# Performance work log

Hardware: AMD Instinct MI355X
Metric: run time of the kernel (lower is better)

## Reference

```python
import jax, jax.numpy as jnp
import numpy as np
from jax.scipy.linalg import expm

LATENT, HID, OMEGA, TRANZ, K = 64, 40, 9, 3, 262144


def _linear_params(key, out_d, in_d):
    # equinox Linear default init: U(-1/sqrt(in), 1/sqrt(in)) for weight and bias
    lim = 1.0 / np.sqrt(in_d)
    kw, kb = jax.random.split(key)
    W = jax.random.uniform(kw, (out_d, in_d), minval=-lim, maxval=lim, dtype=jnp.float32)
    b = jax.random.uniform(kb, (out_d,), minval=-lim, maxval=lim, dtype=jnp.float32)
    return W, b


def setup_inputs() -> dict:
    key = jax.random.key(0)
    keys = jax.random.split(key, 7)
    W_o1, b_o1 = _linear_params(keys[0], HID, LATENT)
    W_o2, b_o2 = _linear_params(keys[1], HID, HID)
    W_o3, b_o3 = _linear_params(keys[2], OMEGA, HID)
    W_t1, b_t1 = _linear_params(keys[3], HID, LATENT)
    W_t2, b_t2 = _linear_params(keys[4], HID, HID)
    W_t3, b_t3 = _linear_params(keys[5], TRANZ, HID)
    x = jax.random.normal(keys[6], (LATENT, K), dtype=jnp.float32)
    return {
        "x": x,
        "W_o1": W_o1, "b_o1": b_o1, "W_o2": W_o2, "b_o2": b_o2, "W_o3": W_o3, "b_o3": b_o3,
        "W_t1": W_t1, "b_t1": b_t1, "W_t2": W_t2, "b_t2": b_t2, "W_t3": W_t3, "b_t3": b_t3,
    }


def _exp_omega(omega_flat):
    # omega_flat: (9, K); expm of each column reshaped to 3x3, flattened -> (K, 9)
    f = lambda col: expm(col.reshape(3, 3)).reshape(9)
    return jax.vmap(f, in_axes=1)(omega_flat)


def reference(x, W_o1, b_o1, W_o2, b_o2, W_o3, b_o3,
              W_t1, b_t1, W_t2, b_t2, W_t3, b_t3):
    relu = jax.nn.relu
    # omega branch (note: original applies relu after EVERY layer, incl. last)
    h = relu(W_o1 @ x + b_o1[:, None])
    h = relu(W_o2 @ h + b_o2[:, None])
    omega = relu(W_o3 @ h + b_o3[:, None])          # (9, K)
    rotation = _exp_omega(omega).T                   # (9, K)
    # translation branch
    t = relu(W_t1 @ x + b_t1[:, None])
    t = relu(W_t2 @ t + b_t2[:, None])
    translation = relu(W_t3 @ t + b_t3[:, None])     # (3, K)
    return (omega, rotation, translation)
```

## Files before the change

kernel.cpp:

```cpp
#include <hip/hip_runtime.h>
#include <hip/hip_bf16.h>

#define KC 262144

typedef __attribute__((ext_vector_type(8))) short bf16x8;
typedef __attribute__((ext_vector_type(4))) float f32x4;
typedef unsigned short u16;
typedef unsigned int u32;

__device__ __forceinline__ u16 f2bf(float f) {
    u32 u = __float_as_uint(f);
    return (u16)((u + 0x7fffu + ((u >> 16) & 1u)) >> 16);
}
__device__ __forceinline__ u32 pk2(float a, float b) {
    return (u32)f2bf(a) | ((u32)f2bf(b) << 16);
}
__device__ __forceinline__ float bf2f(u32 h) {
    return __uint_as_float(h << 16);
}

__global__ __launch_bounds__(256) void prep(
    const float* __restrict__ Wo1, const float* __restrict__ bo1,
    const float* __restrict__ Wo2, const float* __restrict__ bo2,
    const float* __restrict__ Wo3, const float* __restrict__ bo3,
    const float* __restrict__ Wt1, const float* __restrict__ bt1,
    const float* __restrict__ Wt2, const float* __restrict__ bt2,
    const float* __restrict__ Wt3, const float* __restrict__ bt3,
    u16* __restrict__ ws)
{
    u16* W1s = ws;
    u16* W2s = ws + 5120;
    u16* W3s = ws + 12800;
    float* b1s = (float*)(ws + 14336);
    const int t0 = blockIdx.x * 256 + threadIdx.x;
    const int NT = gridDim.x * 256;

    for (int i = t0; i < 5120; i += NT) {
        int r = i >> 6, k = i & 63;
        float v = (r < 40) ? Wo1[r * 64 + k] : Wt1[(r - 40) * 64 + k];
        W1s[i] = f2bf(v);
    }
    for (int i = t0; i < 7680; i += NT) {
        int r = i / 96, k = i - r * 96;
        float v = 0.f;
        if (r < 40) {
            if (k < 40) v = Wo2[r * 40 + k];
            else if (k == 80) v = bo2[r];
        } else {
            int rr = r - 40;
            if (k >= 40 && k < 80) v = Wt2[rr * 40 + (k - 40)];
            else if (k == 80) v = bt2[rr];
        }
        W2s[i] = f2bf(v);
    }
    for (int i = t0; i < 1536; i += NT) {
        int r = i / 96, k = i - r * 96;
        float v = 0.f;
        if (r < 9) {
            if (k < 40) v = Wo3[r * 40 + k];
            else if (k == 80) v = bo3[r];
        } else if (r < 12) {
            int rr = r - 9;
            if (k >= 40 && k < 80) v = Wt3[rr * 40 + (k - 40)];
            else if (k == 80) v = bt3[rr];
        }
        W3s[i] = f2bf(v);
    }
    for (int i = t0; i < 80; i += NT)
        b1s[i] = (i < 40) ? bo1[i] : bt1[i - 40];
}

__global__ __launch_bounds__(256, 2) void mlp_mfma(
    const float* __restrict__ x, const u16* __restrict__ ws,
    float* __restrict__ out)
{
    const u16* W1s = ws;
    const u16* W2s = ws + 5120;
    const u16* W3s = ws + 12800;
    const float* b1s = (const float*)(ws + 14336);

    __shared__ u16 hst[4][16][120];
    __shared__ u16 l3s[4][64][18];

    const int tid = threadIdx.x;
    const int wid = tid >> 6;
    const int lane = tid & 63;
    const int g = lane >> 4;
    const int c = lane & 15;
    const int wgid = blockIdx.x * 4 + wid;
    const int cbase = wgid * 64;

    bf16x8 A1[5][2], A3[3];
    f32x4 b1v[5];
#pragma unroll
    for (int m = 0; m < 5; ++m) {
#pragma unroll
        for (int s = 0; s < 2; ++s)
            A1[m][s] = *(const bf16x8*)(W1s + (16 * m + c) * 64 + 32 * s + 8 * g);
        b1v[m] = *(const f32x4*)(b1s + 16 * m + 4 * g);
    }
    bf16x8 A2[5][3];
#pragma unroll
    for (int m = 0; m < 5; ++m)
#pragma unroll
        for (int s = 0; s < 3; ++s)
            if (!(s == 0 && m >= 3))
                A2[m][s] = *(const bf16x8*)(W2s + (16 * m + c) * 96 + 32 * s + 8 * g);
#pragma unroll
    for (int s = 0; s < 3; ++s)
        A3[s] = *(const bf16x8*)(W3s + c * 96 + 32 * s + 8 * g);

    {
        uint2 z;
        z.x = (g == 0) ? 0x00003f80u : 0u;
        z.y = 0u;
        *(uint2*)&hst[wid][c][80 + 4 * g] = z;
    }

    u32 xoff[16];
#pragma unroll
    for (int jj = 0; jj < 16; ++jj) {
        int row = 8 * g + (jj & 7) + 32 * (jj >> 3);
        xoff[jj] = (u32)((row * KC + cbase + c) * 4);
    }
    const char* xb_ = (const char*)x;

#pragma unroll
    for (int t = 0; t < 4; ++t) {
        float xr[16];
#pragma unroll
        for (int jj = 0; jj < 16; ++jj)
            xr[jj] = *(const float*)(xb_ + (xoff[jj] + t * 64));
        bf16x8 xv[2];
#pragma unroll
        for (int s = 0; s < 2; ++s) {
            union { u32 u[4]; bf16x8 v; } uu;
#pragma unroll
            for (int p = 0; p < 4; ++p)
                uu.u[p] = pk2(xr[8 * s + 2 * p], xr[8 * s + 2 * p + 1]);
            xv[s] = uu.v;
        }

        f32x4 a1[5];
#pragma unroll
        for (int m = 0; m < 5; ++m) a1[m] = b1v[m];
#pragma unroll
        for (int s = 0; s < 2; ++s)
#pragma unroll
            for (int m = 0; m < 5; ++m)
                a1[m] = __builtin_amdgcn_mfma_f32_16x16x32_bf16(
                    A1[m][s], xv[s], a1[m], 0, 0, 0);
#pragma unroll
        for (int m = 0; m < 5; ++m) {
            uint2 w;
            w.x = pk2(fmaxf(a1[m][0], 0.f), fmaxf(a1[m][1], 0.f));
            w.y = pk2(fmaxf(a1[m][2], 0.f), fmaxf(a1[m][3], 0.f));
            *(uint2*)&hst[wid][c][16 * m + 4 * g] = w;
        }

        f32x4 a2[5];
#pragma unroll
        for (int m = 0; m < 5; ++m) a2[m] = f32x4{0.f, 0.f, 0.f, 0.f};
#pragma unroll
        for (int s = 0; s < 3; ++s) {
            bf16x8 hb = *(const bf16x8*)&hst[wid][c][32 * s + 8 * g];
#pragma unroll
            for (int m = 0; m < 5; ++m)
                if (!(s == 0 && m >= 3))
                    a2[m] = __builtin_amdgcn_mfma_f32_16x16x32_bf16(
                        A2[m][s], hb, a2[m], 0, 0, 0);
        }
#pragma unroll
        for (int m = 0; m < 5; ++m) {
            uint2 w;
            w.x = pk2(fmaxf(a2[m][0], 0.f), fmaxf(a2[m][1], 0.f));
            w.y = pk2(fmaxf(a2[m][2], 0.f), fmaxf(a2[m][3], 0.f));
            *(uint2*)&hst[wid][c][16 * m + 4 * g] = w;
        }

        f32x4 a3 = f32x4{0.f, 0.f, 0.f, 0.f};
#pragma unroll
        for (int s = 0; s < 3; ++s) {
            bf16x8 hb = *(const bf16x8*)&hst[wid][c][32 * s + 8 * g];
            a3 = __builtin_amdgcn_mfma_f32_16x16x32_bf16(
                A3[s], hb, a3, 0, 0, 0);
        }
        {
            uint2 w;
            w.x = pk2(fmaxf(a3[0], 0.f), fmaxf(a3[1], 0.f));
            w.y = pk2(fmaxf(a3[2], 0.f), fmaxf(a3[3], 0.f));
            *(uint2*)&l3s[wid][16 * t + c][4 * g] = w;
        }
    }

    {
        uint4 q0 = *(const uint4*)&l3s[wid][lane][0];
        uint2 q1 = *(const uint2*)&l3s[wid][lane][8];
        float om[9];
        om[0] = bf2f(q0.x & 0xffffu); om[1] = bf2f(q0.x >> 16);
        om[2] = bf2f(q0.y & 0xffffu); om[3] = bf2f(q0.y >> 16);
        om[4] = bf2f(q0.z & 0xffffu); om[5] = bf2f(q0.z >> 16);
        om[6] = bf2f(q0.w & 0xffffu); om[7] = bf2f(q0.w >> 16);
        om[8] = bf2f(q1.x & 0xffffu);
        float tr0 = bf2f(q1.x >> 16);
        float tr1 = bf2f(q1.y & 0xffffu);
        float tr2 = bf2f(q1.y >> 16);

        const size_t ob = (size_t)cbase + lane;
#pragma unroll
        for (int j = 0; j < 9; ++j)
            out[(size_t)j * KC + ob] = om[j];
        out[(size_t)18 * KC + ob] = tr0;
        out[(size_t)19 * KC + ob] = tr1;
        out[(size_t)20 * KC + ob] = tr2;

        float B[9];
#pragma unroll
        for (int i = 0; i < 9; ++i) B[i] = om[i] * (1.0f / 32.0f);
        float T[9] = {1.f, 0.f, 0.f, 0.f, 1.f, 0.f, 0.f, 0.f, 1.f};
#pragma unroll
        for (int m = 9; m >= 1; --m) {
            float U[9];
#pragma unroll
            for (int rr = 0; rr < 3; ++rr)
#pragma unroll
                for (int cc = 0; cc < 3; ++cc)
                    U[rr * 3 + cc] = B[rr * 3 + 0] * T[0 * 3 + cc]
                                   + B[rr * 3 + 1] * T[1 * 3 + cc]
                                   + B[rr * 3 + 2] * T[2 * 3 + cc];
            const float s = 1.0f / (float)m;
#pragma unroll
            for (int i = 0; i < 9; ++i)
                T[i] = U[i] * s + ((i == 0 || i == 4 || i == 8) ? 1.0f : 0.0f);
        }
#pragma unroll
        for (int q = 0; q < 5; ++q) {
            float U[9];
#pragma unroll
            for (int rr = 0; rr < 3; ++rr)
#pragma unroll
                for (int cc = 0; cc < 3; ++cc)
                    U[rr * 3 + cc] = T[rr * 3 + 0] * T[0 * 3 + cc]
                                   + T[rr * 3 + 1] * T[1 * 3 + cc]
                                   + T[rr * 3 + 2] * T[2 * 3 + cc];
#pragma unroll
            for (int i = 0; i < 9; ++i) T[i] = U[i];
        }
#pragma unroll
        for (int j = 0; j < 9; ++j)
            out[(size_t)(9 + j) * KC + ob] = T[j];
    }
}

extern "C" void kernel_launch(void* const* d_in, const int* in_sizes, int n_in,
                              void* d_out, int out_size, void* d_ws, size_t ws_size,
                              hipStream_t stream) {
    const float* x   = (const float*)d_in[0];
    const float* Wo1 = (const float*)d_in[1];
    const float* bo1 = (const float*)d_in[2];
    const float* Wo2 = (const float*)d_in[3];
    const float* bo2 = (const float*)d_in[4];
    const float* Wo3 = (const float*)d_in[5];
    const float* bo3 = (const float*)d_in[6];
    const float* Wt1 = (const float*)d_in[7];
    const float* bt1 = (const float*)d_in[8];
    const float* Wt2 = (const float*)d_in[9];
    const float* bt2 = (const float*)d_in[10];
    const float* Wt3 = (const float*)d_in[11];
    const float* bt3 = (const float*)d_in[12];

    u16* ws = (u16*)d_ws;
    float* out = (float*)d_out;

    hipLaunchKernelGGL(prep, dim3(16), dim3(256), 0, stream,
                       Wo1, bo1, Wo2, bo2, Wo3, bo3,
                       Wt1, bt1, Wt2, bt2, Wt3, bt3, ws);
    hipLaunchKernelGGL(mlp_mfma, dim3(1024), dim3(256), 0, stream,
                       x, ws, out);
}
```

Measured before the change: 34.41 us.

## Stage x through LDS with float4 loads and shuffle layer-3 outputs

Replaces the per-lane scalar 4-byte strided loads of x with coalesced float4 global loads staged into a shared slab, from which the MFMA B operands are gathered. Layer-3 results are now redistributed across lanes with warp shuffles instead of an extra LDS buffer, and the hidden-state buffer aliases the x staging slab. The hand-written bf16 rounding is swapped for the library conversion. The aim is wider memory transactions and a smaller LDS footprint, at the cost of extra LDS traffic, shuffle instructions and more registers held live.

```diff
diff --git a/kernel.cpp b/kernel.cpp
--- a/kernel.cpp
+++ b/kernel.cpp
@@ -13,7 +13,9 @@
     return (u16)((u + 0x7fffu + ((u >> 16) & 1u)) >> 16);
 }
 __device__ __forceinline__ u32 pk2(float a, float b) {
-    return (u32)f2bf(a) | ((u32)f2bf(b) << 16);
+    u16 lo = __bfloat16_as_ushort(__float2bfloat16(a));
+    u16 hi = __bfloat16_as_ushort(__float2bfloat16(b));
+    return (u32)lo | ((u32)hi << 16);
 }
 __device__ __forceinline__ float bf2f(u32 h) {
     return __uint_as_float(h << 16);
@@ -79,8 +81,7 @@
     const u16* W3s = ws + 12800;
     const float* b1s = (const float*)(ws + 14336);
 
-    __shared__ u16 hst[4][16][120];
-    __shared__ u16 l3s[4][64][18];
+    __shared__ float slab[4][64 * 36];
 
     const int tid = threadIdx.x;
     const int wid = tid >> 6;
@@ -90,6 +91,9 @@
     const int wgid = blockIdx.x * 4 + wid;
     const int cbase = wgid * 64;
 
+    float* xstage = &slab[wid][0];
+    u16* hstp = (u16*)&slab[wid][0];
+
     bf16x8 A1[5][2], A3[3];
     f32x4 b1v[5];
 #pragma unroll
@@ -110,101 +114,129 @@
     for (int s = 0; s < 3; ++s)
         A3[s] = *(const bf16x8*)(W3s + c * 96 + 32 * s + 8 * g);
 
+    const char* gbase = (const char*)x
+        + ((size_t)(lane >> 3) * KC + (size_t)(cbase + 4 * (lane & 7))) * 4;
+    const int wb = (lane >> 3) * 36 + 4 * (lane & 7);
+
+    u32 w0[4], w1[4];
+
+#pragma unroll
+    for (int ch = 0; ch < 2; ++ch) {
+        float4 G[8];
+#pragma unroll
+        for (int i = 0; i < 8; ++i)
+            G[i] = *(const float4*)(gbase + (size_t)i * 8 * KC * 4 + ch * 128);
+#pragma unroll
+        for (int i = 0; i < 8; ++i)
+            *(float4*)&xstage[wb + i * 288] = G[i];
+
+        bf16x8 xv[2][2];
+#pragma unroll
+        for (int tl = 0; tl < 2; ++tl)
+#pragma unroll
+            for (int s = 0; s < 2; ++s) {
+                union { u32 u[4]; bf16x8 v; } uu;
+#pragma unroll
+                for (int p = 0; p < 4; ++p) {
+                    float lo = xstage[(8 * g + 32 * s + 2 * p) * 36 + 16 * tl + c];
+                    float hi = xstage[(8 * g + 32 * s + 2 * p + 1) * 36 + 16 * tl + c];
+                    uu.u[p] = pk2(lo, hi);
+                }
+                xv[tl][s] = uu.v;
+            }
+
+        {
+            uint2 z;
+            z.x = (g == 0) ? 0x00003f80u : 0u;
+            z.y = 0u;
+            *(uint2*)&hstp[c * 120 + 80 + 4 * g] = z;
+        }
+
+#pragma unroll
+        for (int tl = 0; tl < 2; ++tl) {
+            const int gt = 2 * ch + tl;
+
+            f32x4 a1[5];
+#pragma unroll
+            for (int m = 0; m < 5; ++m) a1[m] = b1v[m];
+#pragma unroll
+            for (int s = 0; s < 2; ++s)
+#pragma unroll
+                for (int m = 0; m < 5; ++m)
+                    a1[m] = __builtin_amdgcn_mfma_f32_16x16x32_bf16(
+                        A1[m][s], xv[tl][s], a1[m], 0, 0, 0);
+#pragma unroll
+            for (int m = 0; m < 5; ++m) {
+                uint2 w;
+                w.x = pk2(fmaxf(a1[m][0], 0.f), fmaxf(a1[m][1], 0.f));
+                w.y = pk2(fmaxf(a1[m][2], 0.f), fmaxf(a1[m][3], 0.f));
+                *(uint2*)&hstp[c * 120 + 16 * m + 4 * g] = w;
+            }
+
+            f32x4 a2[5];
+#pragma unroll
+            for (int m = 0; m < 5; ++m) a2[m] = f32x4{0.f, 0.f, 0.f, 0.f};
+#pragma unroll
+            for (int s = 0; s < 3; ++s) {
+                bf16x8 hb = *(const bf16x8*)&hstp[c * 120 + 32 * s + 8 * g];
+#pragma unroll
+                for (int m = 0; m < 5; ++m)
+                    if (!(s == 0 && m >= 3))
+                        a2[m] = __builtin_amdgcn_mfma_f32_16x16x32_bf16(
+                            A2[m][s], hb, a2[m], 0, 0, 0);
+            }
+#pragma unroll
+            for (int m = 0; m < 5; ++m) {
+                uint2 w;
+                w.x = pk2(fmaxf(a2[m][0], 0.f), fmaxf(a2[m][1], 0.f));
+                w.y = pk2(fmaxf(a2[m][2], 0.f), fmaxf(a2[m][3], 0.f));
+                *(uint2*)&hstp[c * 120 + 16 * m + 4 * g] = w;
+            }
+
+            f32x4 a3 = f32x4{0.f, 0.f, 0.f, 0.f};
+#pragma unroll
+            for (int s = 0; s < 3; ++s) {
+                bf16x8 hb = *(const bf16x8*)&hstp[c * 120 + 32 * s + 8 * g];
+                a3 = __builtin_amdgcn_mfma_f32_16x16x32_bf16(
+                    A3[s], hb, a3, 0, 0, 0);
+            }
+            w0[gt] = pk2(fmaxf(a3[0], 0.f), fmaxf(a3[1], 0.f));
+            w1[gt] = pk2(fmaxf(a3[2], 0.f), fmaxf(a3[3], 0.f));
+        }
+    }
+
     {
-        uint2 z;
-        z.x = (g == 0) ? 0x00003f80u : 0u;
-        z.y = 0u;
-        *(uint2*)&hst[wid][c][80 + 4 * g] = z;
-    }
-
-    u32 xoff[16];
-#pragma unroll
-    for (int jj = 0; jj < 16; ++jj) {
-        int row = 8 * g + (jj & 7) + 32 * (jj >> 3);
-        xoff[jj] = (u32)((row * KC + cbase + c) * 4);
-    }
-    const char* xb_ = (const char*)x;
-
-#pragma unroll
-    for (int t = 0; t < 4; ++t) {
-        float xr[16];
-#pragma unroll
-        for (int jj = 0; jj < 16; ++jj)
-            xr[jj] = *(const float*)(xb_ + (xoff[jj] + t * 64));
-        bf16x8 xv[2];
-#pragma unroll
-        for (int s = 0; s < 2; ++s) {
-            union { u32 u[4]; bf16x8 v; } uu;
-#pragma unroll
-            for (int p = 0; p < 4; ++p)
-                uu.u[p] = pk2(xr[8 * s + 2 * p], xr[8 * s + 2 * p + 1]);
-            xv[s] = uu.v;
-        }
-
-        f32x4 a1[5];
-#pragma unroll
-        for (int m = 0; m < 5; ++m) a1[m] = b1v[m];
-#pragma unroll
-        for (int s = 0; s < 2; ++s)
-#pragma unroll
-            for (int m = 0; m < 5; ++m)
-                a1[m] = __builtin_amdgcn_mfma_f32_16x16x32_bf16(
-                    A1[m][s], xv[s], a1[m], 0, 0, 0);
-#pragma unroll
-        for (int m = 0; m < 5; ++m) {
-            uint2 w;
-            w.x = pk2(fmaxf(a1[m][0], 0.f), fmaxf(a1[m][1], 0.f));
-            w.y = pk2(fmaxf(a1[m][2], 0.f), fmaxf(a1[m][3], 0.f));
-            *(uint2*)&hst[wid][c][16 * m + 4 * g] = w;
-        }
-
-        f32x4 a2[5];
-#pragma unroll
-        for (int m = 0; m < 5; ++m) a2[m] = f32x4{0.f, 0.f, 0.f, 0.f};
-#pragma unroll
-        for (int s = 0; s < 3; ++s) {
-            bf16x8 hb = *(const bf16x8*)&hst[wid][c][32 * s + 8 * g];
-#pragma unroll
-            for (int m = 0; m < 5; ++m)
-                if (!(s == 0 && m >= 3))
-                    a2[m] = __builtin_amdgcn_mfma_f32_16x16x32_bf16(
-                        A2[m][s], hb, a2[m], 0, 0, 0);
-        }
-#pragma unroll
-        for (int m = 0; m < 5; ++m) {
-            uint2 w;
-            w.x = pk2(fmaxf(a2[m][0], 0.f), fmaxf(a2[m][1], 0.f));
-            w.y = pk2(fmaxf(a2[m][2], 0.f), fmaxf(a2[m][3], 0.f));
-            *(uint2*)&hst[wid][c][16 * m + 4 * g] = w;
-        }
-
-        f32x4 a3 = f32x4{0.f, 0.f, 0.f, 0.f};
-#pragma unroll
-        for (int s = 0; s < 3; ++s) {
-            bf16x8 hb = *(const bf16x8*)&hst[wid][c][32 * s + 8 * g];
-            a3 = __builtin_amdgcn_mfma_f32_16x16x32_bf16(
-                A3[s], hb, a3, 0, 0, 0);
-        }
-        {
-            uint2 w;
-            w.x = pk2(fmaxf(a3[0], 0.f), fmaxf(a3[1], 0.f));
-            w.y = pk2(fmaxf(a3[2], 0.f), fmaxf(a3[3], 0.f));
-            *(uint2*)&l3s[wid][16 * t + c][4 * g] = w;
-        }
-    }
-
-    {
-        uint4 q0 = *(const uint4*)&l3s[wid][lane][0];
-        uint2 q1 = *(const uint2*)&l3s[wid][lane][8];
+        const int T = lane >> 4;
+        const int cp = lane & 15;
+        const int s0 = cp, s1 = 16 + cp, s2 = 32 + cp;
+
+        auto selT = [&](u32 v0, u32 v1, u32 v2, u32 v3) -> u32 {
+            u32 lo = (T & 1) ? v1 : v0;
+            u32 hi = (T & 1) ? v3 : v2;
+            return (T & 2) ? hi : lo;
+        };
+        u32 q0 = selT((u32)__shfl((int)w0[0], s0), (u32)__shfl((int)w0[1], s0),
+                      (u32)__shfl((int)w0[2], s0), (u32)__shfl((int)w0[3], s0));
+        u32 q1 = selT((u32)__shfl((int)w1[0], s0), (u32)__shfl((int)w1[1], s0),
+                      (u32)__shfl((int)w1[2], s0), (u32)__shfl((int)w1[3], s0));
+        u32 q2 = selT((u32)__shfl((int)w0[0], s1), (u32)__shfl((int)w0[1], s1),
+                      (u32)__shfl((int)w0[2], s1), (u32)__shfl((int)w0[3], s1));
+        u32 q3 = selT((u32)__shfl((int)w1[0], s1), (u32)__shfl((int)w1[1], s1),
+                      (u32)__shfl((int)w1[2], s1), (u32)__shfl((int)w1[3], s1));
+        u32 q4 = selT((u32)__shfl((int)w0[0], s2), (u32)__shfl((int)w0[1], s2),
+                      (u32)__shfl((int)w0[2], s2), (u32)__shfl((int)w0[3], s2));
+        u32 q5 = selT((u32)__shfl((int)w1[0], s2), (u32)__shfl((int)w1[1], s2),
+                      (u32)__shfl((int)w1[2], s2), (u32)__shfl((int)w1[3], s2));
+
         float om[9];
-        om[0] = bf2f(q0.x & 0xffffu); om[1] = bf2f(q0.x >> 16);
-        om[2] = bf2f(q0.y & 0xffffu); om[3] = bf2f(q0.y >> 16);
-        om[4] = bf2f(q0.z & 0xffffu); om[5] = bf2f(q0.z >> 16);
-        om[6] = bf2f(q0.w & 0xffffu); om[7] = bf2f(q0.w >> 16);
-        om[8] = bf2f(q1.x & 0xffffu);
-        float tr0 = bf2f(q1.x >> 16);
-        float tr1 = bf2f(q1.y & 0xffffu);
-        float tr2 = bf2f(q1.y >> 16);
+        om[0] = bf2f(q0 & 0xffffu); om[1] = bf2f(q0 >> 16);
+        om[2] = bf2f(q1 & 0xffffu); om[3] = bf2f(q1 >> 16);
+        om[4] = bf2f(q2 & 0xffffu); om[5] = bf2f(q2 >> 16);
+        om[6] = bf2f(q3 & 0xffffu); om[7] = bf2f(q3 >> 16);
+        om[8] = bf2f(q4 & 0xffffu);
+        float tr0 = bf2f(q4 >> 16);
+        float tr1 = bf2f(q5 & 0xffffu);
+        float tr2 = bf2f(q5 >> 16);
 
         const size_t ob = (size_t)cbase + lane;
 #pragma unroll
@@ -217,7 +249,7 @@
         float B[9];
 #pragma unroll
         for (int i = 0; i < 9; ++i) B[i] = om[i] * (1.0f / 32.0f);
-        float T[9] = {1.f, 0.f, 0.f, 0.f, 1.f, 0.f, 0.f, 0.f, 1.f};
+        float T9[9] = {1.f, 0.f, 0.f, 0.f, 1.f, 0.f, 0.f, 0.f, 1.f};
 #pragma unroll
         for (int m = 9; m >= 1; --m) {
             float U[9];
@@ -225,13 +257,13 @@
             for (int rr = 0; rr < 3; ++rr)
 #pragma unroll
                 for (int cc = 0; cc < 3; ++cc)
-                    U[rr * 3 + cc] = B[rr * 3 + 0] * T[0 * 3 + cc]
-                                   + B[rr * 3 + 1] * T[1 * 3 + cc]
-                                   + B[rr * 3 + 2] * T[2 * 3 + cc];
+                    U[rr * 3 + cc] = B[rr * 3 + 0] * T9[0 * 3 + cc]
+                                   + B[rr * 3 + 1] * T9[1 * 3 + cc]
+                                   + B[rr * 3 + 2] * T9[2 * 3 + cc];
             const float s = 1.0f / (float)m;
 #pragma unroll
             for (int i = 0; i < 9; ++i)
-                T[i] = U[i] * s + ((i == 0 || i == 4 || i == 8) ? 1.0f : 0.0f);
+                T9[i] = U[i] * s + ((i == 0 || i == 4 || i == 8) ? 1.0f : 0.0f);
         }
 #pragma unroll
         for (int q = 0; q < 5; ++q) {
@@ -240,15 +272,15 @@
             for (int rr = 0; rr < 3; ++rr)
 #pragma unroll
                 for (int cc = 0; cc < 3; ++cc)
-                    U[rr * 3 + cc] = T[rr * 3 + 0] * T[0 * 3 + cc]
-                                   + T[rr * 3 + 1] * T[1 * 3 + cc]
-                                   + T[rr * 3 + 2] * T[2 * 3 + cc];
-#pragma unroll
-            for (int i = 0; i < 9; ++i) T[i] = U[i];
+                    U[rr * 3 + cc] = T9[rr * 3 + 0] * T9[0 * 3 + cc]
+                                   + T9[rr * 3 + 1] * T9[1 * 3 + cc]
+                                   + T9[rr * 3 + 2] * T9[2 * 3 + cc];
+#pragma unroll
+            for (int i = 0; i < 9; ++i) T9[i] = U[i];
         }
 #pragma unroll
         for (int j = 0; j < 9; ++j)
-            out[(size_t)(9 + j) * KC + ob] = T[j];
+            out[(size_t)(9 + j) * KC + ob] = T9[j];
     }
 }
 
```

Result: slower. 35.59 us (+3.4%).
